# Kernel tuning notes

Measured on AMD Instinct MI355X. Metric: run time of the kernel, lower is better.

Reference implementation:

```python
import jax, jax.numpy as jnp
import numpy as np
from jax import lax

B, N, C_FEAT = 16, 32768, 128
NPOINT = 2048
BIG = 1e10  # initial 'infinite' distance, matches torch's 1e10


def farthest_point_sample(xyz, npoint):
    """xyz: [B,N,3] -> indices [B,npoint] via iterative FPS.
    Deterministic start at index 0 (original uses a random start index)."""
    b, n, c = xyz.shape

    def step(carry, _):
        distance, farthest = carry                      # [B,N], [B]
        centroid = jnp.take_along_axis(
            xyz, farthest[:, None, None], axis=1)       # [B,1,3]
        dist = jnp.sum((xyz - centroid) ** 2, axis=-1)  # [B,N]
        distance = jnp.minimum(distance, dist)          # running min dist to chosen set
        new_farthest = jnp.argmax(distance, axis=-1)    # [B]
        return (distance, new_farthest), farthest

    init = (jnp.full((b, n), BIG, xyz.dtype), jnp.zeros((b,), jnp.int32))
    _, idxs = lax.scan(step, init, None, length=npoint)  # [npoint, B]
    return idxs.T                                        # [B, npoint]


def index_points(points, idx):
    """points: [B,N,D], idx: [B,S] -> [B,S,D] gather."""
    return jnp.take_along_axis(points, idx[:, :, None], axis=1)


def setup_inputs() -> dict:
    key = jax.random.key(0)
    k1, k2 = jax.random.split(key)
    xyz = jax.random.normal(k1, (B, N, 3), dtype=jnp.float32)
    features = jax.random.normal(k2, (B, N, C_FEAT), dtype=jnp.float32)
    return {"xyz": xyz, "features": features, "npoint": NPOINT}


def reference(xyz, features, npoint):
    fps_idx = farthest_point_sample(xyz, npoint)   # [B,npoint]
    new_xyz = index_points(xyz, fps_idx)           # [B,npoint,3]
    new_features = index_points(features, fps_idx) # [B,npoint,C]
    return (new_xyz, new_features)
```

## Files before the change

kernel.cpp:

```cpp
#include <hip/hip_runtime.h>

#define BATCH   16
#define NPTS    32768
#define NPOINT  2048
#define C_FEAT  128
#define NSEG    512
#define NTH     1024
#define NW      16


__device__ __forceinline__ unsigned part4(unsigned v) {
  return (v & 1u) | ((v & 2u) << 2) | ((v & 4u) << 4) | ((v & 8u) << 6);
}
__device__ __forceinline__ int morton(float x, float y, float z) {
  const unsigned qx = (unsigned)min(15, max(0, (int)((x + 4.0f) * 2.0f)));
  const unsigned qy = (unsigned)min(15, max(0, (int)((y + 4.0f) * 2.0f)));
  const unsigned qz = (unsigned)min(15, max(0, (int)((z + 4.0f) * 2.0f)));
  return (int)(part4(qx) | (part4(qy) << 1) | (part4(qz) << 2));
}

__device__ __forceinline__ unsigned long long u64max(unsigned long long a,
                                                     unsigned long long b) {
  return a > b ? a : b;
}

__global__ __launch_bounds__(NTH) void sort_kernel(
    const float* __restrict__ xyz, float4* __restrict__ pts,
    int* __restrict__ pos0) {
  const int b = blockIdx.x, t = threadIdx.x, lane = t & 63;
  const float* __restrict__ base = xyz + (size_t)b * NPTS * 3;
  __shared__ unsigned bins[4096];
  __shared__ unsigned wsum[NW];

  for (int i = t; i < 4096; i += NTH) bins[i] = 0u;
  __syncthreads();
  for (int k = 0; k < 32; ++k) {
    const int p = k * NTH + t;
    atomicAdd(&bins[morton(base[p*3], base[p*3+1], base[p*3+2])], 1u);
  }
  __syncthreads();

  unsigned c0 = bins[4*t], c1 = bins[4*t+1], c2 = bins[4*t+2], c3 = bins[4*t+3];
  const unsigned mysum = c0 + c1 + c2 + c3;
  unsigned acc = mysum;
#pragma unroll
  for (int d = 1; d < 64; d <<= 1) {
    unsigned n = __shfl_up(acc, d);
    if (lane >= d) acc += n;
  }
  if (lane == 63) wsum[t >> 6] = acc;
  __syncthreads();
  unsigned woff = 0;
  for (int w = 0; w < (t >> 6); ++w) woff += wsum[w];
  unsigned run = woff + acc - mysum;
  bins[4*t]   = run; run += c0;
  bins[4*t+1] = run; run += c1;
  bins[4*t+2] = run; run += c2;
  bins[4*t+3] = run;
  __syncthreads();

  float4* __restrict__ pb = pts + (size_t)b * NPTS;
  for (int k = 0; k < 32; ++k) {
    const int p = k * NTH + t;
    const float x = base[p*3], y = base[p*3+1], z = base[p*3+2];
    const unsigned pos = atomicAdd(&bins[morton(x, y, z)], 1u);
    pb[pos] = make_float4(x, y, z, __int_as_float(p));
    if (p == 0) pos0[b] = (int)pos;
  }
}

__global__ __launch_bounds__(NTH) void fps_kernel(
    const float4* __restrict__ pts_g, const int* __restrict__ pos0,
    int* __restrict__ fps_idx) {
  const int b = blockIdx.x, t = threadIdx.x, lane = t & 63, w = t >> 6;
  const float4* __restrict__ P = pts_g + (size_t)b * NPTS;

  __shared__ float              dmin[NPTS];
  __shared__ float              sb[6][NSEG];
  __shared__ unsigned long long pack[NSEG];
  __shared__ unsigned long long s_red[2][8];
  __shared__ unsigned short     wl[NSEG];
  __shared__ int                s_cnt[2];

  for (int r = 0; r < 32; ++r) {
    const int seg = w * 32 + r;
    const int i = seg * 64 + lane;
    const float4 q = P[i];
    dmin[i] = 1e10f;
    float xl = q.x, xh = q.x, yl = q.y, yh = q.y, zl = q.z, zh = q.z;
    unsigned k = ((unsigned)__float_as_int(q.w) << 15) | (unsigned)i;
#pragma unroll
    for (int off = 32; off > 0; off >>= 1) {
      xl = fminf(xl, __shfl_xor(xl, off)); xh = fmaxf(xh, __shfl_xor(xh, off));
      yl = fminf(yl, __shfl_xor(yl, off)); yh = fmaxf(yh, __shfl_xor(yh, off));
      zl = fminf(zl, __shfl_xor(zl, off)); zh = fmaxf(zh, __shfl_xor(zh, off));
      k  = min(k, (unsigned)__shfl_xor((int)k, off));
    }
    if (lane == 0) {
      sb[0][seg] = xl; sb[1][seg] = xh;
      sb[2][seg] = yl; sb[3][seg] = yh;
      sb[4][seg] = zl; sb[5][seg] = zh;
      pack[seg] = ((unsigned long long)__float_as_uint(1e10f) << 32) |
                  (unsigned long long)(0x3FFFFFFFu - k);
    }
  }
  if (t == 0) { s_cnt[0] = 0; s_cnt[1] = 0; }
  __syncthreads();

  int far = 0;
  const float4 q0 = P[pos0[b]];
  float cx = q0.x, cy = q0.y, cz = q0.z;

  for (int s = 0; s < NPOINT; ++s) {
    if (t == 0) fps_idx[b * NPOINT + s] = far;
    if (t == NTH - 1) s_cnt[(s + 1) & 1] = 0;

    if (t < NSEG) {
      const unsigned long long pk = pack[t];
      const float cm = __uint_as_float((unsigned)(pk >> 32));
      const float ddx = fmaxf(fmaxf(sb[0][t] - cx, cx - sb[1][t]), 0.0f);
      const float ddy = fmaxf(fmaxf(sb[2][t] - cy, cy - sb[3][t]), 0.0f);
      const float ddz = fmaxf(fmaxf(sb[4][t] - cz, cz - sb[5][t]), 0.0f);
      const float r2 = ddx * ddx + ddy * ddy + ddz * ddz;
      const bool need = !(r2 * 0.999f > cm);
      const unsigned long long bal = __ballot(need);
      int wb = 0;
      if (lane == 0 && bal != 0ull)
        wb = atomicAdd(&s_cnt[s & 1], (int)__popcll(bal));
      wb = __shfl(wb, 0);
      if (need) {
        const unsigned long long ltm = (1ull << lane) - 1ull;
        wl[wb + (int)__popcll(bal & ltm)] = (unsigned short)t;
      }
    }
    __syncthreads();

    const int C = s_cnt[s & 1];
    for (int e = w; e < C; e += NW) {
      const int seg = (int)wl[e];
      const int i = seg * 64 + lane;
      const float4 q = P[i];
      const float dx = q.x - cx, dy = q.y - cy, dz = q.z - cz;
      const float d = __builtin_fmaf(dz, dz, __builtin_fmaf(dy, dy, dx * dx));
      const float nd = fminf(dmin[i], d);
      dmin[i] = nd;
      float vm = nd;
      unsigned bk = ((unsigned)__float_as_int(q.w) << 15) | (unsigned)i;
#pragma unroll
      for (int off = 32; off > 0; off >>= 1) {
        const float    ov  = __shfl_xor(vm, off);
        const unsigned obk = (unsigned)__shfl_xor((int)bk, off);
        if (ov > vm || (ov == vm && obk < bk)) { vm = ov; bk = obk; }
      }
      if (lane == 0)
        pack[seg] = ((unsigned long long)__float_as_uint(vm) << 32) |
                    (unsigned long long)(0x3FFFFFFFu - bk);
    }
    __syncthreads();

    if (t < NSEG) {
      unsigned long long p = pack[t];
#pragma unroll
      for (int off = 32; off > 0; off >>= 1) {
        const unsigned lo = (unsigned)p, hi = (unsigned)(p >> 32);
        const unsigned olo = (unsigned)__shfl_xor((int)lo, off);
        const unsigned ohi = (unsigned)__shfl_xor((int)hi, off);
        p = u64max(p, ((unsigned long long)ohi << 32) | olo);
      }
      if (lane == 0) s_red[s & 1][w] = p;
    }
    __syncthreads();

    unsigned long long p = s_red[s & 1][0];
#pragma unroll
    for (int j = 1; j < 8; ++j) p = u64max(p, s_red[s & 1][j]);
    const unsigned kwin = 0x3FFFFFFFu - (unsigned)(p & 0x3FFFFFFFu);
    far = (int)(kwin >> 15);
    const float4 qn = P[(int)(kwin & 0x7FFFu)];
    cx = qn.x; cy = qn.y; cz = qn.z;
  }
}

__global__ __launch_bounds__(256) void gather_kernel(
    const float* __restrict__ xyz, const float* __restrict__ feat,
    const int* __restrict__ fps_idx, float* __restrict__ out) {
  const int lane = threadIdx.x & 31;
  const int sub  = threadIdx.x >> 5;
  const int row  = blockIdx.x * 8 + sub;
  const int b    = row >> 11;
  const int src  = fps_idx[row];

  const float4* __restrict__ f =
      reinterpret_cast<const float4*>(feat + ((size_t)b * NPTS + src) * C_FEAT);
  float4* __restrict__ o =
      reinterpret_cast<float4*>(out + (size_t)BATCH * NPOINT * 3 +
                                (size_t)row * C_FEAT);
  o[lane] = f[lane];
  if (lane < 3) {
    out[(size_t)row * 3 + lane] = xyz[((size_t)b * NPTS + src) * 3 + lane];
  }
}

extern "C" void kernel_launch(void* const* d_in, const int* in_sizes, int n_in,
                              void* d_out, int out_size, void* d_ws, size_t ws_size,
                              hipStream_t stream) {
  (void)in_sizes; (void)n_in; (void)out_size; (void)ws_size;
  const float* xyz  = (const float*)d_in[0];
  const float* feat = (const float*)d_in[1];
  float* out = (float*)d_out;

  char* ws = (char*)d_ws;
  int*    fps_idx = (int*)ws;
  int*    pos0    = (int*)(ws + (1u << 17));
  float4* pts     = (float4*)(ws + (1u << 20));

  sort_kernel<<<BATCH, NTH, 0, stream>>>(xyz, pts, pos0);
  fps_kernel<<<BATCH, NTH, 0, stream>>>(pts, pos0, fps_idx);
  gather_kernel<<<(BATCH * NPOINT) / 8, 256, 0, stream>>>(xyz, feat, fps_idx, out);
}
```

Baseline: 4.761 ms.

## Fold per-step argmax reduction into every wave and cache winner coords in LDS

Removes the dedicated block-wide reduction phase, with its per-wave partial array and extra barrier, from each FPS iteration. Instead, every wave redundantly reduces all 512 segment maxima straight from shared memory at the top of the step. Each segment's current winner coordinates are kept in a new shared array, so the next centroid comes from LDS rather than a dependent global load. The sort kernel no longer records the start position. The trade is eight LDS loads plus one shuffle reduction in every wave per step, in exchange for one fewer barrier and no global load on the serial critical path.

```diff
diff --git a/kernel.cpp b/kernel.cpp
--- a/kernel.cpp
+++ b/kernel.cpp
@@ -25,8 +25,7 @@
 }
 
 __global__ __launch_bounds__(NTH) void sort_kernel(
-    const float* __restrict__ xyz, float4* __restrict__ pts,
-    int* __restrict__ pos0) {
+    const float* __restrict__ xyz, float4* __restrict__ pts) {
   const int b = blockIdx.x, t = threadIdx.x, lane = t & 63;
   const float* __restrict__ base = xyz + (size_t)b * NPTS * 3;
   __shared__ unsigned bins[4096];
@@ -65,20 +64,18 @@
     const float x = base[p*3], y = base[p*3+1], z = base[p*3+2];
     const unsigned pos = atomicAdd(&bins[morton(x, y, z)], 1u);
     pb[pos] = make_float4(x, y, z, __int_as_float(p));
-    if (p == 0) pos0[b] = (int)pos;
   }
 }
 
 __global__ __launch_bounds__(NTH) void fps_kernel(
-    const float4* __restrict__ pts_g, const int* __restrict__ pos0,
-    int* __restrict__ fps_idx) {
+    const float4* __restrict__ pts_g, int* __restrict__ fps_idx) {
   const int b = blockIdx.x, t = threadIdx.x, lane = t & 63, w = t >> 6;
   const float4* __restrict__ P = pts_g + (size_t)b * NPTS;
 
   __shared__ float              dmin[NPTS];
   __shared__ float              sb[6][NSEG];
+  __shared__ float              cand[3][NSEG];
   __shared__ unsigned long long pack[NSEG];
-  __shared__ unsigned long long s_red[2][8];
   __shared__ unsigned short     wl[NSEG];
   __shared__ int                s_cnt[2];
 
@@ -87,8 +84,10 @@
     const int i = seg * 64 + lane;
     const float4 q = P[i];
     dmin[i] = 1e10f;
+    const unsigned mykey =
+        ((unsigned)__float_as_int(q.w) << 15) | (unsigned)i;
     float xl = q.x, xh = q.x, yl = q.y, yh = q.y, zl = q.z, zh = q.z;
-    unsigned k = ((unsigned)__float_as_int(q.w) << 15) | (unsigned)i;
+    unsigned k = mykey;
 #pragma unroll
     for (int off = 32; off > 0; off >>= 1) {
       xl = fminf(xl, __shfl_xor(xl, off)); xh = fmaxf(xh, __shfl_xor(xh, off));
@@ -103,15 +102,29 @@
       pack[seg] = ((unsigned long long)__float_as_uint(1e10f) << 32) |
                   (unsigned long long)(0x3FFFFFFFu - k);
     }
+    if (mykey == k) {
+      cand[0][seg] = q.x; cand[1][seg] = q.y; cand[2][seg] = q.z;
+    }
   }
   if (t == 0) { s_cnt[0] = 0; s_cnt[1] = 0; }
   __syncthreads();
 
-  int far = 0;
-  const float4 q0 = P[pos0[b]];
-  float cx = q0.x, cy = q0.y, cz = q0.z;
-
   for (int s = 0; s < NPOINT; ++s) {
+    unsigned long long p = pack[lane];
+#pragma unroll
+    for (int j = 1; j < 8; ++j) p = u64max(p, pack[lane + j * 64]);
+#pragma unroll
+    for (int off = 32; off > 0; off >>= 1) {
+      const unsigned lo = (unsigned)p, hi = (unsigned)(p >> 32);
+      const unsigned olo = (unsigned)__shfl_xor((int)lo, off);
+      const unsigned ohi = (unsigned)__shfl_xor((int)hi, off);
+      p = u64max(p, ((unsigned long long)ohi << 32) | olo);
+    }
+    const unsigned kwin = 0x3FFFFFFFu - (unsigned)(p & 0x3FFFFFFFu);
+    const int far  = (int)(kwin >> 15);
+    const int segw = (int)((kwin & 0x7FFFu) >> 6);
+    const float cx = cand[0][segw], cy = cand[1][segw], cz = cand[2][segw];
+
     if (t == 0) fps_idx[b * NPOINT + s] = far;
     if (t == NTH - 1) s_cnt[(s + 1) & 1] = 0;
 
@@ -145,7 +158,9 @@
       const float nd = fminf(dmin[i], d);
       dmin[i] = nd;
       float vm = nd;
-      unsigned bk = ((unsigned)__float_as_int(q.w) << 15) | (unsigned)i;
+      const unsigned mykey =
+          ((unsigned)__float_as_int(q.w) << 15) | (unsigned)i;
+      unsigned bk = mykey;
 #pragma unroll
       for (int off = 32; off > 0; off >>= 1) {
         const float    ov  = __shfl_xor(vm, off);
@@ -155,29 +170,11 @@
       if (lane == 0)
         pack[seg] = ((unsigned long long)__float_as_uint(vm) << 32) |
                     (unsigned long long)(0x3FFFFFFFu - bk);
+      if (mykey == bk) {
+        cand[0][seg] = q.x; cand[1][seg] = q.y; cand[2][seg] = q.z;
+      }
     }
     __syncthreads();
-
-    if (t < NSEG) {
-      unsigned long long p = pack[t];
-#pragma unroll
-      for (int off = 32; off > 0; off >>= 1) {
-        const unsigned lo = (unsigned)p, hi = (unsigned)(p >> 32);
-        const unsigned olo = (unsigned)__shfl_xor((int)lo, off);
-        const unsigned ohi = (unsigned)__shfl_xor((int)hi, off);
-        p = u64max(p, ((unsigned long long)ohi << 32) | olo);
-      }
-      if (lane == 0) s_red[s & 1][w] = p;
-    }
-    __syncthreads();
-
-    unsigned long long p = s_red[s & 1][0];
-#pragma unroll
-    for (int j = 1; j < 8; ++j) p = u64max(p, s_red[s & 1][j]);
-    const unsigned kwin = 0x3FFFFFFFu - (unsigned)(p & 0x3FFFFFFFu);
-    far = (int)(kwin >> 15);
-    const float4 qn = P[(int)(kwin & 0x7FFFu)];
-    cx = qn.x; cy = qn.y; cz = qn.z;
   }
 }
 
@@ -211,10 +208,9 @@
 
   char* ws = (char*)d_ws;
   int*    fps_idx = (int*)ws;
-  int*    pos0    = (int*)(ws + (1u << 17));
   float4* pts     = (float4*)(ws + (1u << 20));
 
-  sort_kernel<<<BATCH, NTH, 0, stream>>>(xyz, pts, pos0);
-  fps_kernel<<<BATCH, NTH, 0, stream>>>(pts, pos0, fps_idx);
+  sort_kernel<<<BATCH, NTH, 0, stream>>>(xyz, pts);
+  fps_kernel<<<BATCH, NTH, 0, stream>>>(pts, fps_idx);
   gather_kernel<<<(BATCH * NPOINT) / 8, 256, 0, stream>>>(xyz, feat, fps_idx, out);
 }
```

Result: slower. 5.206 ms (+9.3%).
